# Kernel optimization log

Hardware: AMD Instinct MI355X
Metric: run time of the kernel (lower is better)

Reference implementation:

```python
import jax, jax.numpy as jnp
import numpy as np

D_MODEL = 768
N_HEADS = 12
D_HEAD = 64
WINDOW = 16
LOOK_BACK = 1
IGNORE = -1.0e6


def look_around(x, backward=LOOK_BACK, forward=0, pad_value=0):
    # x: (b, n_windows, w, ...) -> (b, n_windows, w*(backward+forward+1), ...)
    n = x.shape[1]
    pad = [(0, 0)] * x.ndim
    pad[1] = (backward, forward)
    px = jnp.pad(x, pad, constant_values=pad_value)
    return jnp.concatenate([px[:, i:i + n] for i in range(backward + forward + 1)], axis=2)


def setup_inputs() -> dict:
    key = jax.random.key(0)
    k1, k2, k3 = jax.random.split(key, 3)
    B, T = 2, 2048
    x = jax.random.normal(k1, (B, T, D_MODEL), dtype=jnp.float32)
    W_abcde = jax.random.normal(k2, (D_MODEL, 5 * N_HEADS * D_HEAD), dtype=jnp.float32) * (1.0 / np.sqrt(D_MODEL))
    b_abcde = jnp.zeros((5 * N_HEADS * D_HEAD,), dtype=jnp.float32)
    W_O = jax.random.normal(k3, (N_HEADS * D_HEAD, D_MODEL), dtype=jnp.float32) * (1.0 / np.sqrt(N_HEADS * D_HEAD))
    b_O = jnp.zeros((D_MODEL,), dtype=jnp.float32)
    return {"x": x, "W_abcde": W_abcde, "b_abcde": b_abcde, "W_O": W_O, "b_O": b_O}


def reference(x, W_abcde, b_abcde, W_O, b_O):
    B, T, _ = x.shape
    w = WINDOW
    nw = T // w
    Ww = w * (LOOK_BACK + 1)  # look-around window length

    abcde = x @ W_abcde + b_abcde                                    # (B,T,5*H*D)
    abcde = abcde.reshape(B, T, 5, N_HEADS, D_HEAD).transpose(2, 0, 3, 1, 4)  # (5,B,H,T,D)
    a, b, c, d, e = [t.reshape(B * N_HEADS, nw, w, D_HEAD) for t in abcde]
    a_l, b_l, d_l, e_l = (look_around(t) for t in (a, b, d, e))       # (BH,nw,Ww,D)

    # causal mask, same construction as get_causal_mask (pad_value=0)
    seq = jnp.arange(T).reshape(1, nw, w)
    bb = look_around(seq)                                            # (1,nw,Ww)
    # mask[n,m,l] = (seq_n < bb_l) | (bb_l <= bb_m)
    mask = (seq[..., :, None, None] < bb[..., None, None, :]) | (bb[..., None, None, :] <= bb[..., None, :, None])

    # third-order attention scores: (BH, nw, w, Ww, Ww)
    scores = jnp.einsum('bnwd,bnmd,bnld->bnwml', c, a_l, b_l)
    scores = jnp.where(mask, IGNORE, scores)
    scores = jnp.where(scores == 0, IGNORE, scores)
    probs = jax.nn.softmax((scores / D_HEAD).reshape(B * N_HEADS, nw, w, Ww * Ww), axis=-1)
    probs = probs.reshape(scores.shape)

    z = jnp.einsum('bnwml,bnmd->bnwd', probs, d_l) + jnp.einsum('bnwml,bnld->bnwd', probs, e_l)
    z = z.reshape(B, N_HEADS, nw, w, D_HEAD).transpose(0, 2, 3, 1, 4).reshape(B, T, N_HEADS * D_HEAD)
    return z @ W_O + b_O
```

## Files before the change

kernel.cpp:

```cpp
#include <hip/hip_runtime.h>

#define T_SEQ   2048
#define NHEADS  12
#define DHEAD   64
#define WIN     16
#define WW      32
#define NWIN    128
#define DMODEL  768
#define NABCDE  3840
#define IGNORE_V (-1.0e6f)
#define PAD_K   72
#define PAD_R   52
#define L2E64   0.022542110013890053f
#define IGN_SC  (-22542.110013890053f)

typedef float f32x4 __attribute__((ext_vector_type(4)));
typedef _Float16 f16x8 __attribute__((ext_vector_type(8)));

__device__ __forceinline__ short f2h(float f) {
    union { _Float16 h; short s; } u;
    u.h = (_Float16)f;
    return u.s;
}

__device__ __forceinline__ void gload_lds16(const short* g, short* l) {
    __builtin_amdgcn_global_load_lds(
        (const __attribute__((address_space(1))) void*)g,
        (__attribute__((address_space(3))) void*)l,
        16, 0, 0);
}

__global__ __launch_bounds__(256) void prep_kernel(
    const float* __restrict__ x, const float* __restrict__ W_abcde,
    const float* __restrict__ W_O,
    short* __restrict__ xh, short* __restrict__ Wt, short* __restrict__ WOt)
{
    __shared__ float tile[32][33];
    const int blk = blockIdx.x;
    const int tid = threadIdx.x;

    if (blk < 1536) {
        int i = (blk * 256 + tid) * 8;
        float4 a = *reinterpret_cast<const float4*>(&x[i]);
        float4 b = *reinterpret_cast<const float4*>(&x[i + 4]);
        union { short s[8]; uint4 u; } r;
        r.s[0] = f2h(a.x); r.s[1] = f2h(a.y); r.s[2] = f2h(a.z); r.s[3] = f2h(a.w);
        r.s[4] = f2h(b.x); r.s[5] = f2h(b.y); r.s[6] = f2h(b.z); r.s[7] = f2h(b.w);
        *reinterpret_cast<uint4*>(&xh[i]) = r.u;
        return;
    }
    const float* W; short* Wo; int N, bx, by;
    if (blk < 4416) {
        int t = blk - 1536;
        W = W_abcde; Wo = Wt; N = NABCDE;
        bx = (t % 120) * 32; by = (t / 120) * 32;
    } else {
        int t = blk - 4416;
        W = W_O; Wo = WOt; N = DMODEL;
        bx = (t % 24) * 32; by = (t / 24) * 32;
    }
    const int tx = tid & 31, ty = tid >> 5;
#pragma unroll
    for (int r = 0; r < 32; r += 8)
        tile[ty + r][tx] = W[(size_t)(by + ty + r) * N + bx + tx];
    __syncthreads();
#pragma unroll
    for (int r = 0; r < 32; r += 8)
        Wo[(size_t)(bx + ty + r) * DMODEL + by + tx] = f2h(tile[tx][ty + r]);
}

__global__ __launch_bounds__(512, 2) void gemm1_kernel(
    const short* __restrict__ A, const short* __restrict__ Bt,
    const float* __restrict__ bias, short* __restrict__ C,
    int M, int N, int K)
{
    __shared__ short LT[4][2][8192];

    const int tid  = threadIdx.x;
    const int wave = tid >> 6;
    const int lane = tid & 63;

    int bid = blockIdx.x;
    int t = (bid & 7) * 30 + (bid >> 3);
    const int bm = (t / 15) * 256;
    const int bn = (t % 15) * 256;

    const int wr = wave >> 2;
    const int wc = wave & 3;
    const int fm = lane & 15;
    const int ko = lane >> 4;
    const int kswz = ko ^ ((lane >> 2) & 3);
    const int w32 = wave * 32;

    const int srow = lane >> 2;
    const int scc  = ((lane & 3) ^ ((lane >> 4) & 3)) * 8;
    const short* gA[2]; const short* gB[2];
#pragma unroll
    for (int j = 0; j < 2; ++j) {
        gA[j] = A  + (size_t)(bm + w32 + j * 16 + srow) * K + scc;
        gB[j] = Bt + (size_t)(bn + w32 + j * 16 + srow) * K + scc;
    }

    f32x4 acc[8][4];
#pragma unroll
    for (int mi = 0; mi < 8; ++mi)
#pragma unroll
        for (int ni = 0; ni < 4; ++ni) acc[mi][ni] = (f32x4){0.f, 0.f, 0.f, 0.f};

#pragma unroll
    for (int kt = 0; kt < 3; ++kt) {
#pragma unroll
        for (int j = 0; j < 2; ++j) {
            gload_lds16(gA[j] + kt * 32, &LT[kt][0][(w32 + j * 16) * 32]);
            gload_lds16(gB[j] + kt * 32, &LT[kt][1][(w32 + j * 16) * 32]);
        }
    }

    const int NKT = K >> 5;
    const int nkm = NKT - 3;

#define G1_STEP(KB, VMC, DOSTAGE, KS)                                          \
    {                                                                          \
        asm volatile("s_waitcnt vmcnt(" #VMC ")" ::: "memory");                \
        __builtin_amdgcn_s_barrier();                                          \
        asm volatile("" ::: "memory");                                         \
        if (DOSTAGE) {                                                         \
            int sb_ = (KS) & 3;                                                \
            _Pragma("unroll")                                                  \
            for (int j = 0; j < 2; ++j) {                                      \
                gload_lds16(gA[j] + (KS) * 32, &LT[sb_][0][(w32 + j * 16) * 32]); \
                gload_lds16(gB[j] + (KS) * 32, &LT[sb_][1][(w32 + j * 16) * 32]); \
            }                                                                  \
        }                                                                      \
        const short* Ab_ = &LT[(KB)][0][0];                                    \
        const short* Bb_ = &LT[(KB)][1][0];                                    \
        f16x8 af_[8], bf_[4];                                                  \
        _Pragma("unroll")                                                      \
        for (int mi = 0; mi < 8; ++mi)                                         \
            af_[mi] = *reinterpret_cast<const f16x8*>(                         \
                &Ab_[(wr * 128 + mi * 16 + fm) * 32 + kswz * 8]);              \
        _Pragma("unroll")                                                      \
        for (int ni = 0; ni < 4; ++ni)                                         \
            bf_[ni] = *reinterpret_cast<const f16x8*>(                         \
                &Bb_[(wc * 64 + ni * 16 + fm) * 32 + kswz * 8]);               \
        __builtin_amdgcn_s_setprio(1);                                         \
        _Pragma("unroll")                                                      \
        for (int mi = 0; mi < 8; ++mi)                                         \
            _Pragma("unroll")                                                  \
            for (int ni = 0; ni < 4; ++ni)                                     \
                acc[mi][ni] = __builtin_amdgcn_mfma_f32_16x16x32_f16(          \
                    af_[mi], bf_[ni], acc[mi][ni], 0, 0, 0);                   \
        __builtin_amdgcn_s_setprio(0);                                         \
    }

    for (int k = 0; k < nkm; ++k) {
        G1_STEP(k & 3, 8, true, k + 3);
    }
    G1_STEP(nkm & 3, 8, false, 0);
    G1_STEP((nkm + 1) & 3, 4, false, 0);
    G1_STEP((nkm + 2) & 3, 0, false, 0);
#undef G1_STEP

    float bv[4];
#pragma unroll
    for (int ni = 0; ni < 4; ++ni)
        bv[ni] = bias[bn + wc * 64 + ni * 16 + fm];

    short* cb = &LT[0][0][0];
#pragma unroll
    for (int half = 0; half < 2; ++half) {
        __syncthreads();
        if (wr == half) {
#pragma unroll
            for (int mi = 0; mi < 8; ++mi) {
#pragma unroll
                for (int r = 0; r < 4; ++r) {
                    int lrow = mi * 16 + ko * 4 + r;
#pragma unroll
                    for (int ni = 0; ni < 4; ++ni)
                        cb[lrow * 256 + wc * 64 + ni * 16 + fm] =
                            f2h(acc[mi][ni][r] + bv[ni]);
                }
            }
        }
        __syncthreads();
#pragma unroll
        for (int q = 0; q < 8; ++q) {
            int f = tid + q * 512;
            int row = f >> 5, c16 = (f & 31) * 8;
            *reinterpret_cast<uint4*>(
                &C[(size_t)(bm + half * 128 + row) * N + bn + c16]) =
                *reinterpret_cast<const uint4*>(&cb[row * 256 + c16]);
        }
    }
}

__global__ __launch_bounds__(256) void gemm_h16_64(
    const short* __restrict__ A, const short* __restrict__ Bt,
    const float* __restrict__ bias, float* __restrict__ C,
    int M, int N, int K)
{
    __shared__ short As[2][64 * 32];
    __shared__ short Bs[2][64 * 32];

    const int tid  = threadIdx.x;
    const int wave = tid >> 6;
    const int lane = tid & 63;
    const int bm = blockIdx.y * 64;
    const int bn = blockIdx.x * 64;

    const int st_row = lane >> 2;
    const int st_col = (lane & 3) * 8;
    const int fr_m = lane & 15;
    const int fr_k = (lane >> 4) * 8;
    const int wm = wave * 16;

    const short* gsrc[4];
    short* ldst[4];
#pragma unroll
    for (int j = 0; j < 4; ++j) {
        int c = wave * 4 + j;
        if (c < 8) {
            int kt = c >> 2, rg = c & 3;
            gsrc[j] = A + (size_t)(bm + rg * 16 + st_row) * K + kt * 32 + st_col;
            ldst[j] = &As[kt][(rg * 16) * 32];
        } else {
            int cb = c - 8;
            int kt = cb >> 2, rg = cb & 3;
            gsrc[j] = Bt + (size_t)(bn + rg * 16 + st_row) * K + kt * 32 + st_col;
            ldst[j] = &Bs[kt][(rg * 16) * 32];
        }
    }

    f32x4 acc[4];
#pragma unroll
    for (int ni = 0; ni < 4; ++ni) acc[ni] = (f32x4){0.f, 0.f, 0.f, 0.f};

    for (int k0 = 0; k0 < K; k0 += 64) {
#pragma unroll
        for (int j = 0; j < 4; ++j) gload_lds16(gsrc[j] + k0, ldst[j]);
        __syncthreads();

#pragma unroll
        for (int kt = 0; kt < 2; ++kt) {
            f16x8 af = *reinterpret_cast<const f16x8*>(
                &As[kt][(wm + fr_m) * 32 + fr_k]);
#pragma unroll
            for (int ni = 0; ni < 4; ++ni) {
                f16x8 bf = *reinterpret_cast<const f16x8*>(
                    &Bs[kt][(ni * 16 + fr_m) * 32 + fr_k]);
                acc[ni] = __builtin_amdgcn_mfma_f32_16x16x32_f16(
                    af, bf, acc[ni], 0, 0, 0);
            }
        }
        __syncthreads();
    }

    float bv[4];
#pragma unroll
    for (int ni = 0; ni < 4; ++ni)
        bv[ni] = bias[bn + ni * 16 + (lane & 15)];
    int rbase = bm + wm + (lane >> 4) * 4;
#pragma unroll
    for (int r = 0; r < 4; ++r) {
        size_t off = (size_t)(rbase + r) * N + bn + (lane & 15);
#pragma unroll
        for (int ni = 0; ni < 4; ++ni)
            C[off + ni * 16] = acc[ni][r] + bv[ni];
    }
}

__global__ __launch_bounds__(512) void attn_kernel(
    const short* __restrict__ abcde, short* __restrict__ z)
{
    const int bid = blockIdx.x;
    const int blk = (bid & 7) * 192 + (bid >> 3);
    const int jp = blk & 63;
    const int bh = blk >> 6;
    const int b  = bh / NHEADS;
    const int h  = bh % NHEADS;
    const int n0 = jp * 2;

    __shared__ short sc[32 * PAD_K];
    __shared__ short sa[48 * PAD_K];
    __shared__ short sb[48 * PAD_K];
    __shared__ short sdT[64 * PAD_R];
    __shared__ short seT[64 * PAD_R];
    __shared__ short epA[32 * PAD_K];
    __shared__ float sinv[32];

    const int tid = threadIdx.x;
    const size_t rowbase = ((size_t)b * T_SEQ) * NABCDE;
    const int hd = h * DHEAD;

    if (tid < 256) {
        int row = tid >> 3, ch = (tid & 7) * 8;
        *reinterpret_cast<uint4*>(&sc[row * PAD_K + ch]) =
            *reinterpret_cast<const uint4*>(
                &abcde[rowbase + (size_t)(n0 * WIN + row) * NABCDE + 2 * DMODEL + hd + ch]);
    }
    if (tid < 384) {
        int row = tid >> 3, ch = (tid & 7) * 8;
        int t = n0 * WIN - WIN + row;
        uint4 va = {0u, 0u, 0u, 0u}, vb = va, vd = va, ve = va;
        if (t >= 0) {
            size_t base = rowbase + (size_t)t * NABCDE + hd + ch;
            va = *reinterpret_cast<const uint4*>(&abcde[base + 0 * DMODEL]);
            vb = *reinterpret_cast<const uint4*>(&abcde[base + 1 * DMODEL]);
            vd = *reinterpret_cast<const uint4*>(&abcde[base + 3 * DMODEL]);
            ve = *reinterpret_cast<const uint4*>(&abcde[base + 4 * DMODEL]);
        }
        *reinterpret_cast<uint4*>(&sa[row * PAD_K + ch]) = va;
        *reinterpret_cast<uint4*>(&sb[row * PAD_K + ch]) = vb;
        union { uint4 u; short s[8]; } Dv, Ev;
        Dv.u = vd; Ev.u = ve;
#pragma unroll
        for (int q = 0; q < 8; ++q) {
            sdT[(ch + q) * PAD_R + row] = Dv.s[q];
            seT[(ch + q) * PAD_R + row] = Ev.s[q];
        }
    }
    __syncthreads();

    const int wv = tid >> 6;
    const int w  = wv >> 2;
    const int wvl = wv & 3;
    const int n  = n0 + w;
    const int lane = tid & 63;
    const int lc = lane & 15;
    const int ko = lane >> 4;
    const int lb = w * 16;
    const int ew = w * 16;

    f16x8 cfrag[2];
    f16x8 bfrag[2][2];
#pragma unroll
    for (int kt = 0; kt < 2; ++kt) {
        cfrag[kt] = *reinterpret_cast<const f16x8*>(
            &sc[(ew + wvl * 4 + (lc & 3)) * PAD_K + kt * 32 + ko * 8]) * (_Float16)L2E64;
        bfrag[0][kt] = *reinterpret_cast<const f16x8*>(&sb[(lb + lc) * PAD_K + kt * 32 + ko * 8]);
        bfrag[1][kt] = *reinterpret_cast<const f16x8*>(&sb[(lb + 16 + lc) * PAD_K + kt * 32 + ko * 8]);
    }

    f32x4 acc[8][2];
#pragma unroll
    for (int mt = 0; mt < 8; ++mt) {
        acc[mt][0] = (f32x4){0.f, 0.f, 0.f, 0.f};
        acc[mt][1] = (f32x4){0.f, 0.f, 0.f, 0.f};
    }
    __builtin_amdgcn_s_setprio(1);
#pragma unroll
    for (int mt = 0; mt < 8; ++mt) {
#pragma unroll
        for (int kt = 0; kt < 2; ++kt) {
            f16x8 ar = *reinterpret_cast<const f16x8*>(
                &sa[(lb + mt * 4 + (lc >> 2)) * PAD_K + kt * 32 + ko * 8]);
            f16x8 pa = cfrag[kt] * ar;
            acc[mt][0] = __builtin_amdgcn_mfma_f32_16x16x32_f16(pa, bfrag[0][kt], acc[mt][0], 0, 0, 0);
            acc[mt][1] = __builtin_amdgcn_mfma_f32_16x16x32_f16(pa, bfrag[1][kt], acc[mt][1], 0, 0, 0);
        }
    }
    __builtin_amdgcn_s_setprio(0);

    if (n != 0) {
#pragma unroll
        for (int lt = 0; lt < 2; ++lt) {
            const int l = lt * 16 + lc;
#pragma unroll
            for (int mt = 0; mt < 8; ++mt) {
                const bool mgt = l > (mt * 4 + ko);
#pragma unroll
                for (int reg = 0; reg < 4; ++reg) {
                    const bool keep = mgt && (wvl * 4 + reg + WIN >= l);
                    float p = __builtin_amdgcn_exp2f(acc[mt][lt][reg]);
                    acc[mt][lt][reg] = keep ? p : 0.0f;
                }
            }
        }
    } else {
        int bbl_h[2]; bool keepL[2][4];
#pragma unroll
        for (int lt = 0; lt < 2; ++lt) {
            int l = lt * 16 + lc;
            bbl_h[lt] = (l < WIN) ? 0 : (l - WIN);
#pragma unroll
            for (int reg = 0; reg < 4; ++reg)
                keepL[lt][reg] = (wvl * 4 + reg) >= bbl_h[lt];
        }
#pragma unroll
        for (int mt = 0; mt < 8; ++mt) {
            int m = mt * 4 + ko;
            int bbm = (m < WIN) ? 0 : (m - WIN);
#pragma unroll
            for (int lt = 0; lt < 2; ++lt) {
                bool mgt = bbl_h[lt] > bbm;
#pragma unroll
                for (int reg = 0; reg < 4; ++reg) {
                    float s = acc[mt][lt][reg];
                    if (!(keepL[lt][reg] && mgt) || s == 0.0f)
                        acc[mt][lt][reg] = IGN_SC;
                }
            }
        }
        float mx[4] = {-3.4e38f, -3.4e38f, -3.4e38f, -3.4e38f};
#pragma unroll
        for (int mt = 0; mt < 8; ++mt)
#pragma unroll
            for (int lt = 0; lt < 2; ++lt)
#pragma unroll
                for (int reg = 0; reg < 4; ++reg)
                    mx[reg] = fmaxf(mx[reg], acc[mt][lt][reg]);
#pragma unroll
        for (int reg = 0; reg < 4; ++reg) {
#pragma unroll
            for (int off = 1; off < 64; off <<= 1)
                mx[reg] = fmaxf(mx[reg], __shfl_xor(mx[reg], off, 64));
        }
#pragma unroll
        for (int mt = 0; mt < 8; ++mt)
#pragma unroll
            for (int lt = 0; lt < 2; ++lt)
#pragma unroll
                for (int reg = 0; reg < 4; ++reg)
                    acc[mt][lt][reg] = __builtin_amdgcn_exp2f(
                        acc[mt][lt][reg] - mx[reg]);
    }

    float plv[2][4];
#pragma unroll
    for (int lt = 0; lt < 2; ++lt) {
#pragma unroll
        for (int reg = 0; reg < 4; ++reg) {
            float p = acc[0][lt][reg];
#pragma unroll
            for (int mt = 1; mt < 8; ++mt) p += acc[mt][lt][reg];
            p += __shfl_xor(p, 16, 64);
            p += __shfl_xor(p, 32, 64);
            plv[lt][reg] = p;
        }
        float w1  = (ko & 1) ? plv[lt][1] : plv[lt][0];
        float w2 = (ko & 1) ? plv[lt][3] : plv[lt][2];
        float ww = (ko & 2) ? w2 : w1;
        epA[(ew + wvl * 4 + ko) * PAD_K + 32 + lt * 16 + lc] = f2h(ww);
    }

    {
        float s[4];
#pragma unroll
        for (int reg = 0; reg < 4; ++reg) {
            float t = plv[0][reg] + plv[1][reg];
            t += __shfl_xor(t, 1, 64);
            t += __shfl_xor(t, 2, 64);
            t += __shfl_xor(t, 4, 64);
            t += __shfl_xor(t, 8, 64);
            s[reg] = t;
        }
        if (lane == 0) {
#pragma unroll
            for (int reg = 0; reg < 4; ++reg) sinv[ew + wvl * 4 + reg] = 1.0f / s[reg];
        }
    }

    {
        float v8[8][4];
#pragma unroll
        for (int mt = 0; mt < 8; ++mt)
#pragma unroll
            for (int reg = 0; reg < 4; ++reg)
                v8[mt][reg] = acc[mt][0][reg] + acc[mt][1][reg];

        const bool s0 = lane & 1, s1 = lane & 2, s2 = lane & 4, s3 = lane & 8;
        float r1[4][4];
#pragma unroll
        for (int m2 = 0; m2 < 4; ++m2)
#pragma unroll
            for (int reg = 0; reg < 4; ++reg) {
                float u = v8[2 * m2][reg], wq = v8[2 * m2 + 1][reg];
                float a = s0 ? wq : u;
                float s = s0 ? u : wq;
                r1[m2][reg] = a + __shfl_xor(s, 1, 64);
            }
        float r2[2][4];
#pragma unroll
        for (int m4 = 0; m4 < 2; ++m4)
#pragma unroll
            for (int reg = 0; reg < 4; ++reg) {
                float u = r1[2 * m4][reg], wq = r1[2 * m4 + 1][reg];
                float a = s1 ? wq : u;
                float s = s1 ? u : wq;
                r2[m4][reg] = a + __shfl_xor(s, 2, 64);
            }
        float r3[4];
#pragma unroll
        for (int reg = 0; reg < 4; ++reg) {
            float u = r2[0][reg], wq = r2[1][reg];
            float a = s2 ? wq : u;
            float s = s2 ? u : wq;
            r3[reg] = a + __shfl_xor(s, 4, 64);
        }
        float a0 = s3 ? r3[1] : r3[0];
        float q0 = s3 ? r3[0] : r3[1];
        float g0 = a0 + __shfl_xor(q0, 8, 64);
        float a1 = s3 ? r3[3] : r3[2];
        float q1 = s3 ? r3[2] : r3[3];
        float g1 = a1 + __shfl_xor(q1, 8, 64);

        int mcol = (lc & 7) * 4 + ko;
        int ib = ew + wvl * 4 + (lc >> 3);
        epA[ib * PAD_K + mcol]       = f2h(g0);
        epA[(ib + 2) * PAD_K + mcol] = f2h(g1);
    }

    const int dd = wvl * 16 + lc;
    f16x8 bd, be;
    {
        const int base = dd * PAD_R + lb + ko * 8;
        union { uint2 u2[2]; f16x8 v; } td, te;
        td.u2[0] = *reinterpret_cast<const uint2*>(&sdT[base]);
        td.u2[1] = *reinterpret_cast<const uint2*>(&sdT[base + 4]);
        te.u2[0] = *reinterpret_cast<const uint2*>(&seT[base]);
        te.u2[1] = *reinterpret_cast<const uint2*>(&seT[base + 4]);
        bd = td.v; be = te.v;
    }
    __syncthreads();

    f16x8 apm = *reinterpret_cast<const f16x8*>(&epA[(ew + lc) * PAD_K + ko * 8]);
    f16x8 apl = *reinterpret_cast<const f16x8*>(&epA[(ew + lc) * PAD_K + 32 + ko * 8]);
    f32x4 zacc = (f32x4){0.f, 0.f, 0.f, 0.f};
    __builtin_amdgcn_s_setprio(1);
    zacc = __builtin_amdgcn_mfma_f32_16x16x32_f16(apm, bd, zacc, 0, 0, 0);
    zacc = __builtin_amdgcn_mfma_f32_16x16x32_f16(apl, be, zacc, 0, 0, 0);
    __builtin_amdgcn_s_setprio(0);

    short* zs = sdT;
#pragma unroll
    for (int reg = 0; reg < 4; ++reg) {
        int i = ew + ko * 4 + reg;
        zs[i * 64 + dd] = f2h(zacc[reg] * sinv[i]);
    }
    __syncthreads();
    {
        int row = tid >> 4;
        int ch  = (tid & 15) * 4;
        *reinterpret_cast<uint2*>(
            &z[((size_t)b * T_SEQ + n0 * WIN + row) * (NHEADS * DHEAD) + hd + ch]) =
            *reinterpret_cast<const uint2*>(&zs[row * 64 + ch]);
    }
}

extern "C" void kernel_launch(void* const* d_in, const int* in_sizes, int n_in,
                              void* d_out, int out_size, void* d_ws, size_t ws_size,
                              hipStream_t stream) {
    const float* x        = (const float*)d_in[0];
    const float* W_abcde  = (const float*)d_in[1];
    const float* b_abcde  = (const float*)d_in[2];
    const float* W_O      = (const float*)d_in[3];
    const float* b_O      = (const float*)d_in[4];
    float* out = (float*)d_out;

    char* ws = (char*)d_ws;
    short* abcde = (short*)ws;
    short* xh    = (short*)(ws + (size_t)31457280);
    short* Wt    = (short*)(ws + (size_t)31457280 + 6291456);
    short* WOt   = (short*)(ws + (size_t)31457280 + 6291456 + 5898240);
    short* zb    = xh;

    const int M = 2 * T_SEQ;

    prep_kernel<<<dim3(4992), dim3(256), 0, stream>>>(
        x, W_abcde, W_O, xh, Wt, WOt);

    gemm1_kernel<<<dim3(240), dim3(512), 0, stream>>>(
        xh, Wt, b_abcde, abcde, M, NABCDE, DMODEL);

    attn_kernel<<<dim3(NHEADS * NWIN), dim3(512), 0, stream>>>(abcde, zb);

    gemm_h16_64<<<dim3(DMODEL / 64, M / 64), dim3(256), 0, stream>>>(
        zb, WOt, b_O, out, M, DMODEL, DMODEL);
}
```

Measured before the change: 146.7 us.

## Shrink gemm1 tiles to 128x128 with 256 threads and XCD-aware supertile mapping

```diff
diff --git a/kernel.cpp b/kernel.cpp
--- a/kernel.cpp
+++ b/kernel.cpp
@@ -69,52 +69,62 @@
         Wo[(size_t)(bx + ty + r) * DMODEL + by + tx] = f2h(tile[tx][ty + r]);
 }
 
-__global__ __launch_bounds__(512, 2) void gemm1_kernel(
+__global__ __launch_bounds__(256) void gemm1_kernel(
     const short* __restrict__ A, const short* __restrict__ Bt,
     const float* __restrict__ bias, short* __restrict__ C,
     int M, int N, int K)
 {
-    __shared__ short LT[4][2][8192];
+    __shared__ short LT[4][8192];
 
     const int tid  = threadIdx.x;
     const int wave = tid >> 6;
     const int lane = tid & 63;
 
     int bid = blockIdx.x;
-    int t = (bid & 7) * 30 + (bid >> 3);
-    const int bm = (t / 15) * 256;
-    const int bn = (t % 15) * 256;
-
-    const int wr = wave >> 2;
-    const int wc = wave & 3;
+    int xcd = bid & 7, t = bid >> 3;
+    int sidx = t / 40, inner = t % 40;
+    int sid = sidx * 8 + xcd;
+    int sy = sid / 3, sx = sid % 3;
+    const int ty = sy * 4 + (inner & 3);
+    const int tx = sx * 10 + (inner >> 2);
+    const int bm = ty * 128;
+    const int bn = tx * 128;
+
+    const int wr = wave >> 1;
+    const int wn = (wave & 1) * 64;
     const int fm = lane & 15;
     const int ko = lane >> 4;
     const int kswz = ko ^ ((lane >> 2) & 3);
-    const int w32 = wave * 32;
 
     const int srow = lane >> 2;
     const int scc  = ((lane & 3) ^ ((lane >> 4) & 3)) * 8;
-    const short* gA[2]; const short* gB[2];
-#pragma unroll
-    for (int j = 0; j < 2; ++j) {
-        gA[j] = A  + (size_t)(bm + w32 + j * 16 + srow) * K + scc;
-        gB[j] = Bt + (size_t)(bn + w32 + j * 16 + srow) * K + scc;
-    }
-
-    f32x4 acc[8][4];
-#pragma unroll
-    for (int mi = 0; mi < 8; ++mi)
+
+    const short* gsrc[4];
+    int loff[4];
+#pragma unroll
+    for (int j = 0; j < 4; ++j) {
+        int c = wave * 4 + j;
+        if (c < 8) {
+            gsrc[j] = A + (size_t)(bm + c * 16 + srow) * K + scc;
+            loff[j] = (c * 16) * 32;
+        } else {
+            int cb = c - 8;
+            gsrc[j] = Bt + (size_t)(bn + cb * 16 + srow) * K + scc;
+            loff[j] = 4096 + (cb * 16) * 32;
+        }
+    }
+
+    f32x4 acc[4][4];
+#pragma unroll
+    for (int mi = 0; mi < 4; ++mi)
 #pragma unroll
         for (int ni = 0; ni < 4; ++ni) acc[mi][ni] = (f32x4){0.f, 0.f, 0.f, 0.f};
 
 #pragma unroll
-    for (int kt = 0; kt < 3; ++kt) {
-#pragma unroll
-        for (int j = 0; j < 2; ++j) {
-            gload_lds16(gA[j] + kt * 32, &LT[kt][0][(w32 + j * 16) * 32]);
-            gload_lds16(gB[j] + kt * 32, &LT[kt][1][(w32 + j * 16) * 32]);
-        }
-    }
+    for (int kt = 0; kt < 3; ++kt)
+#pragma unroll
+        for (int j = 0; j < 4; ++j)
+            gload_lds16(gsrc[j] + kt * 32, &LT[kt][loff[j]]);
 
     const int NKT = K >> 5;
     const int nkm = NKT - 3;
@@ -127,25 +137,22 @@
         if (DOSTAGE) {                                                         \
             int sb_ = (KS) & 3;                                                \
             _Pragma("unroll")                                                  \
-            for (int j = 0; j < 2; ++j) {                                      \
-                gload_lds16(gA[j] + (KS) * 32, &LT[sb_][0][(w32 + j * 16) * 32]); \
-                gload_lds16(gB[j] + (KS) * 32, &LT[sb_][1][(w32 + j * 16) * 32]); \
-            }                                                                  \
+            for (int j = 0; j < 4; ++j)                                        \
+                gload_lds16(gsrc[j] + (KS) * 32, &LT[sb_][loff[j]]);           \
         }                                                                      \
-        const short* Ab_ = &LT[(KB)][0][0];                                    \
-        const short* Bb_ = &LT[(KB)][1][0];                                    \
-        f16x8 af_[8], bf_[4];                                                  \
+        const short* Lb_ = &LT[(KB)][0];                                       \
+        f16x8 af_[4], bf_[4];                                                  \
         _Pragma("unroll")                                                      \
-        for (int mi = 0; mi < 8; ++mi)                                         \
+        for (int mi = 0; mi < 4; ++mi)                                         \
             af_[mi] = *reinterpret_cast<const f16x8*>(                         \
-                &Ab_[(wr * 128 + mi * 16 + fm) * 32 + kswz * 8]);              \
+                &Lb_[(wr * 64 + mi * 16 + fm) * 32 + kswz * 8]);               \
         _Pragma("unroll")                                                      \
         for (int ni = 0; ni < 4; ++ni)                                         \
             bf_[ni] = *reinterpret_cast<const f16x8*>(                         \
-                &Bb_[(wc * 64 + ni * 16 + fm) * 32 + kswz * 8]);               \
+                &Lb_[4096 + (wn + ni * 16 + fm) * 32 + kswz * 8]);             \
         __builtin_amdgcn_s_setprio(1);                                         \
         _Pragma("unroll")                                                      \
-        for (int mi = 0; mi < 8; ++mi)                                         \
+        for (int mi = 0; mi < 4; ++mi)                                         \
             _Pragma("unroll")                                                  \
             for (int ni = 0; ni < 4; ++ni)                                     \
                 acc[mi][ni] = __builtin_amdgcn_mfma_f32_16x16x32_f16(          \
@@ -164,33 +171,33 @@
     float bv[4];
 #pragma unroll
     for (int ni = 0; ni < 4; ++ni)
-        bv[ni] = bias[bn + wc * 64 + ni * 16 + fm];
-
-    short* cb = &LT[0][0][0];
+        bv[ni] = bias[bn + wn + ni * 16 + fm];
+
+    short* cb = &LT[0][0];
 #pragma unroll
     for (int half = 0; half < 2; ++half) {
         __syncthreads();
         if (wr == half) {
 #pragma unroll
-            for (int mi = 0; mi < 8; ++mi) {
+            for (int mi = 0; mi < 4; ++mi) {
 #pragma unroll
                 for (int r = 0; r < 4; ++r) {
-                    int lrow = mi * 16 + ko * 4 + r;
+                    int row = mi * 16 + ko * 4 + r;
 #pragma unroll
                     for (int ni = 0; ni < 4; ++ni)
-                        cb[lrow * 256 + wc * 64 + ni * 16 + fm] =
+                        cb[row * 128 + wn + ni * 16 + fm] =
                             f2h(acc[mi][ni][r] + bv[ni]);
                 }
             }
         }
         __syncthreads();
 #pragma unroll
-        for (int q = 0; q < 8; ++q) {
-            int f = tid + q * 512;
-            int row = f >> 5, c16 = (f & 31) * 8;
+        for (int q = 0; q < 4; ++q) {
+            int f = tid + q * 256;
+            int row = f >> 4, c16 = (f & 15) * 8;
             *reinterpret_cast<uint4*>(
-                &C[(size_t)(bm + half * 128 + row) * N + bn + c16]) =
-                *reinterpret_cast<const uint4*>(&cb[row * 256 + c16]);
+                &C[(size_t)(bm + half * 64 + row) * N + bn + c16]) =
+                *reinterpret_cast<const uint4*>(&cb[row * 128 + c16]);
         }
     }
 }
@@ -570,7 +577,7 @@
     prep_kernel<<<dim3(4992), dim3(256), 0, stream>>>(
         x, W_abcde, W_O, xh, Wt, WOt);
 
-    gemm1_kernel<<<dim3(240), dim3(512), 0, stream>>>(
+    gemm1_kernel<<<dim3(960), dim3(256), 0, stream>>>(
         xh, Wt, b_abcde, abcde, M, NABCDE, DMODEL);
 
     attn_kernel<<<dim3(NHEADS * NWIN), dim3(512), 0, stream>>>(abcde, zb);
```

Result: slower. 154.3 us (+5.2%).
